# Kernel tuning notes

Measured on AMD Instinct MI355X. Metric: run time of the kernel, lower is better.

Reference implementation:

```python
import jax, jax.numpy as jnp
import numpy as np
from jax import lax

V, H, L, F = 50304, 512, 6, 2048
SKIP_INTERVAL = 1
B, S = 4, 1024


def layer_norm(x, w, b, eps=1e-5):
    mu = jnp.mean(x, axis=-1, keepdims=True)
    var = jnp.mean(jnp.square(x - mu), axis=-1, keepdims=True)
    return (x - mu) * lax.rsqrt(var + eps) * w + b


def setup_inputs() -> dict:
    key = jax.random.key(0)
    ks = jax.random.split(key, 8)
    s = 0.02
    return {
        "input_ids": jax.random.randint(ks[0], (B, S), 0, V, dtype=jnp.int64),
        "embed_in": jax.random.normal(ks[1], (V, H), jnp.float32) * s,
        "hp_w": jax.random.normal(ks[2], (H, H), jnp.float32) * s,
        "hp_b": jnp.zeros((H,), jnp.float32),
        "ln_w": jnp.ones((L, H), jnp.float32),
        "ln_b": jnp.zeros((L, H), jnp.float32),
        "W1": jax.random.normal(ks[3], (L, H, F), jnp.float32) * s,
        "b1": jnp.zeros((L, F), jnp.float32),
        "W2": jax.random.normal(ks[4], (L, F, H), jnp.float32) * s,
        "b2": jnp.zeros((L, H), jnp.float32),
        "ln_f_w": jnp.ones((H,), jnp.float32),
        "ln_f_b": jnp.zeros((H,), jnp.float32),
        "embed_out_w": jax.random.normal(ks[5], (V, H), jnp.float32) * s,
    }


def _stack(h, ln_w, ln_b, W1, b1, W2, b2):
    # scan over L layers; each is pre-LN residual MLP: h + gelu(LN(h) @ W1 + b1) @ W2 + b2
    def step(h, p):
        lw, lb, w1, bb1, w2, bb2 = p
        y = layer_norm(h, lw, lb)
        h = h + jnp.dot(jax.nn.gelu(jnp.dot(y, w1) + bb1), w2) + bb2
        return h, None
    h, _ = lax.scan(step, h, (ln_w, ln_b, W1, b1, W2, b2))
    return h


def reference(input_ids, embed_in, hp_w, hp_b, ln_w, ln_b, W1, b1, W2, b2, ln_f_w, ln_f_b, embed_out_w):
    # forward_selective with attention_mask=None and stateless layers is
    # position-independent, so the token loop vectorizes exactly to [B,S,H].
    h = embed_in[input_ids]  # [B,S,H] gather
    h = _stack(h, ln_w, ln_b, W1, b1, W2, b2)
    for _ in range(SKIP_INTERVAL):
        h = jnp.dot(h, hp_w.T) + hp_b  # hidden_proj
        h = _stack(h, ln_w, ln_b, W1, b1, W2, b2)
    normed = layer_norm(h, ln_f_w, ln_f_b)
    logits = jnp.dot(normed, embed_out_w.T)  # [B,S,V]
    final_hidden = h[:, -1, :]  # [B,H]
    return logits, final_hidden
```

## Files before the change

kernel.cpp:

```cpp
#include <hip/hip_runtime.h>
#include <hip/hip_bf16.h>
#include <cstdint>

using bf16 = __hip_bfloat16;
typedef __bf16 bf16x8 __attribute__((ext_vector_type(8)));
typedef float f32x4 __attribute__((ext_vector_type(4)));

constexpr int Hd = 512;
constexpr int Ld = 6;
constexpr int Fd = 2048;
constexpr int Vd = 50304;
constexpr int Md = 4096;

__device__ __forceinline__ unsigned short f2b(float x) {
  return __builtin_bit_cast(unsigned short, __float2bfloat16(x));
}

__device__ __forceinline__ float gelu_tanh(float x) {
  const float c = 0.7978845608028654f;
  float x3 = x * x * x;
  return 0.5f * x * (1.0f + tanhf(c * (x + 0.044715f * x3)));
}

__device__ __forceinline__ void load16_lds(const bf16* g, bf16* l) {
  __builtin_amdgcn_global_load_lds(
      (const __attribute__((address_space(1))) void*)g,
      (__attribute__((address_space(3))) void*)l, 16, 0, 0);
}

__global__ __launch_bounds__(256) void cast8(const float* __restrict__ in,
                                             bf16* __restrict__ out, int n8) {
  int i = blockIdx.x * 256 + threadIdx.x;
  if (i >= n8) return;
  const float4* p = (const float4*)in;
  float4 a = p[2 * i], b = p[2 * i + 1];
  uint4 o = {(unsigned)f2b(a.x) | ((unsigned)f2b(a.y) << 16),
             (unsigned)f2b(a.z) | ((unsigned)f2b(a.w) << 16),
             (unsigned)f2b(b.x) | ((unsigned)f2b(b.y) << 16),
             (unsigned)f2b(b.z) | ((unsigned)f2b(b.w) << 16)};
  ((uint4*)out)[i] = o;
}

__global__ void transpose_cast(const float* __restrict__ in, bf16* __restrict__ out,
                               int R, int C) {
  __shared__ float tile[32][33];
  int l = blockIdx.z;
  in += (size_t)l * R * C;
  out += (size_t)l * R * C;
  int c0 = blockIdx.x * 32, r0 = blockIdx.y * 32;
#pragma unroll
  for (int i = 0; i < 4; i++) {
    int r = r0 + threadIdx.y + i * 8;
    tile[threadIdx.y + i * 8][threadIdx.x] = in[(size_t)r * C + c0 + threadIdx.x];
  }
  __syncthreads();
#pragma unroll
  for (int i = 0; i < 4; i++) {
    int c = c0 + threadIdx.y + i * 8;
    out[(size_t)c * R + r0 + threadIdx.x] = (bf16)tile[threadIdx.x][threadIdx.y + i * 8];
  }
}

__global__ void gather_embed(const int* __restrict__ ids, const float* __restrict__ emb,
                             float* __restrict__ h) {
  int row = blockIdx.x;
  int id = ids[row];
  const float4* src = (const float4*)(emb + (size_t)id * Hd);
  float4* dst = (float4*)(h + (size_t)row * Hd);
  dst[threadIdx.x] = src[threadIdx.x];
}

template <int MODE>
__global__ __launch_bounds__(256) void ln_rows(
    const float* __restrict__ h, const float* __restrict__ p0,
    const float* __restrict__ p1, const float* __restrict__ fb,
    const float* __restrict__ w, const float* __restrict__ b,
    float* __restrict__ hout, bf16* __restrict__ y) {
  int row = blockIdx.x * 4 + (threadIdx.x >> 6);
  int lane = threadIdx.x & 63;
  size_t base = (size_t)row * Hd + lane * 8;
  float xv[8];
  if constexpr (MODE == 0) {
    *(float4*)&xv[0] = *(const float4*)(h + base);
    *(float4*)&xv[4] = *(const float4*)(h + base + 4);
  } else {
    float4 q0 = *(const float4*)(p0 + base), q1 = *(const float4*)(p0 + base + 4);
    float4 r0 = *(const float4*)(p1 + base), r1 = *(const float4*)(p1 + base + 4);
    float4 f0 = *(const float4*)(fb + lane * 8), f1 = *(const float4*)(fb + lane * 8 + 4);
    xv[0] = q0.x + r0.x + f0.x; xv[1] = q0.y + r0.y + f0.y;
    xv[2] = q0.z + r0.z + f0.z; xv[3] = q0.w + r0.w + f0.w;
    xv[4] = q1.x + r1.x + f1.x; xv[5] = q1.y + r1.y + f1.y;
    xv[6] = q1.z + r1.z + f1.z; xv[7] = q1.w + r1.w + f1.w;
    if constexpr (MODE == 1) {
      float4 a0 = *(const float4*)(h + base), a1 = *(const float4*)(h + base + 4);
      xv[0] += a0.x; xv[1] += a0.y; xv[2] += a0.z; xv[3] += a0.w;
      xv[4] += a1.x; xv[5] += a1.y; xv[6] += a1.z; xv[7] += a1.w;
    }
    *(float4*)(hout + base) = make_float4(xv[0], xv[1], xv[2], xv[3]);
    *(float4*)(hout + base + 4) = make_float4(xv[4], xv[5], xv[6], xv[7]);
  }
  float s = 0.f;
#pragma unroll
  for (int j = 0; j < 8; j++) s += xv[j];
#pragma unroll
  for (int off = 1; off < 64; off <<= 1) s += __shfl_xor(s, off);
  float mu = s * (1.0f / 512.0f);
  float s2 = 0.f;
#pragma unroll
  for (int j = 0; j < 8; j++) {
    xv[j] -= mu;
    s2 += xv[j] * xv[j];
  }
#pragma unroll
  for (int off = 1; off < 64; off <<= 1) s2 += __shfl_xor(s2, off);
  float scale = rsqrtf(s2 * (1.0f / 512.0f) + 1e-5f);
  float o[8];
#pragma unroll
  for (int j = 0; j < 8; j++) {
    float wj = w[lane * 8 + j], bj = b[lane * 8 + j];
    o[j] = xv[j] * scale * wj + bj;
  }
  uint4 pk = {(unsigned)f2b(o[0]) | ((unsigned)f2b(o[1]) << 16),
              (unsigned)f2b(o[2]) | ((unsigned)f2b(o[3]) << 16),
              (unsigned)f2b(o[4]) | ((unsigned)f2b(o[5]) << 16),
              (unsigned)f2b(o[6]) | ((unsigned)f2b(o[7]) << 16)};
  *(uint4*)(y + base) = pk;
}

__global__ __launch_bounds__(256) void finish2(
    const float* __restrict__ p0, const float* __restrict__ p1,
    const float* __restrict__ fb, float* __restrict__ h, bf16* __restrict__ hbf) {
  int i = blockIdx.x * 256 + threadIdx.x;
  size_t base = (size_t)i * 8;
  int col = (int)(base & 511);
  float x[8];
#pragma unroll
  for (int j = 0; j < 8; j += 4) {
    float4 a = *(const float4*)(h + base + j);
    float4 q = *(const float4*)(p0 + base + j);
    float4 r = *(const float4*)(p1 + base + j);
    float4 f = *(const float4*)(fb + col + j);
    x[j] = a.x + q.x + r.x + f.x; x[j + 1] = a.y + q.y + r.y + f.y;
    x[j + 2] = a.z + q.z + r.z + f.z; x[j + 3] = a.w + q.w + r.w + f.w;
    *(float4*)(h + base + j) = make_float4(x[j], x[j + 1], x[j + 2], x[j + 3]);
  }
  uint4 pk = {(unsigned)f2b(x[0]) | ((unsigned)f2b(x[1]) << 16),
              (unsigned)f2b(x[2]) | ((unsigned)f2b(x[3]) << 16),
              (unsigned)f2b(x[4]) | ((unsigned)f2b(x[5]) << 16),
              (unsigned)f2b(x[6]) | ((unsigned)f2b(x[7]) << 16)};
  *(uint4*)(hbf + base) = pk;
}

template <int EPI, int BN, bool MSWZ>
__global__ __launch_bounds__(256) void gemm_bt(
    const bf16* __restrict__ A, const bf16* __restrict__ Bt,
    const float* __restrict__ bias, float* __restrict__ outF,
    bf16* __restrict__ outB, int M, int N, int Klen, int lda, int ldb) {
  constexpr int ASZ = 128 * 32;
  constexpr int BSZ = BN * 32;
  constexpr int TILE = ASZ + BSZ;
  __shared__ bf16 lds[3 * TILE];
  const int tid = threadIdx.x;
  const int wave = tid >> 6;
  const int lane = tid & 63;
  constexpr int NF = BN / 32;
  const int wm = (wave >> 1) * 64;
  const int wn = (wave & 1) * (BN / 2);

  int bm, bn;
  if constexpr (MSWZ) {
    const int per = gridDim.x >> 3;
    const int wg = (blockIdx.x & 7) * per + (blockIdx.x >> 3);
    const int nM = M >> 7;
    bm = wg & (nM - 1);
    bn = wg / nM;
  } else {
    bn = blockIdx.x;
    bm = blockIdx.y;
  }
  const int rowA0 = bm * 128;
  const int rowB0 = bn * BN;
  const int k0 = blockIdx.z * Klen;

  const bf16* srcA[2];
#pragma unroll
  for (int r = 0; r < 2; r++) {
    int c = (r * 4 + wave) * 64 + lane;
    srcA[r] = A + (size_t)(rowA0 + (c >> 2)) * lda + k0 + (c & 3) * 8;
  }
  const bf16* srcB[BN / 64];
#pragma unroll
  for (int r = 0; r < BN / 64; r++) {
    int c = (r * 4 + wave) * 64 + lane;
    srcB[r] = Bt + (size_t)(rowB0 + (c >> 2)) * ldb + k0 + (c & 3) * 8;
  }

  f32x4 acc[4][NF];
#pragma unroll
  for (int i = 0; i < 4; i++)
#pragma unroll
    for (int j = 0; j < NF; j++) acc[i][j] = (f32x4){0.f, 0.f, 0.f, 0.f};

  const int fr = lane & 15;
  const int ko = (lane >> 4) * 8;

  auto STAGE = [&](int slot) {
    bf16* dst = lds + slot * TILE;
#pragma unroll
    for (int r = 0; r < 2; r++) {
      load16_lds(srcA[r], dst + (r * 4 + wave) * 512);
      srcA[r] += 32;
    }
#pragma unroll
    for (int r = 0; r < BN / 64; r++) {
      load16_lds(srcB[r], dst + ASZ + (r * 4 + wave) * 512);
      srcB[r] += 32;
    }
  };

  STAGE(0);
  STAGE(1);
  const int nIter = Klen >> 5;
  int cur = 0, stg = 2;
  for (int it = 0; it < nIter; ++it) {
    if (it < nIter - 1) {
      if constexpr (BN == 64)
        asm volatile("s_waitcnt vmcnt(3)" ::: "memory");
      else
        asm volatile("s_waitcnt vmcnt(4)" ::: "memory");
    } else {
      asm volatile("s_waitcnt vmcnt(0)" ::: "memory");
    }
    __builtin_amdgcn_s_barrier();
    __builtin_amdgcn_sched_barrier(0);
    if (it + 2 < nIter) STAGE(stg);
    const bf16* lA = lds + cur * TILE;
    const bf16* lB = lA + ASZ;
    bf16x8 af[4], bfr[NF];
#pragma unroll
    for (int f = 0; f < 4; f++)
      af[f] = *(const bf16x8*)(lA + (wm + f * 16 + fr) * 32 + ko);
#pragma unroll
    for (int f = 0; f < NF; f++)
      bfr[f] = *(const bf16x8*)(lB + (wn + f * 16 + fr) * 32 + ko);
#pragma unroll
    for (int i = 0; i < 4; i++)
#pragma unroll
      for (int j = 0; j < NF; j++)
        acc[i][j] = __builtin_amdgcn_mfma_f32_16x16x32_bf16(af[i], bfr[j], acc[i][j], 0, 0, 0);
    cur = (cur == 2) ? 0 : cur + 1;
    stg = (stg == 2) ? 0 : stg + 1;
  }

  if constexpr (EPI == 4) outF += (size_t)blockIdx.z * M * N;
  const int orow = (lane >> 4) * 4;
  const int ocol = lane & 15;
#pragma unroll
  for (int i = 0; i < 4; i++) {
#pragma unroll
    for (int j = 0; j < NF; j++) {
      int row0 = rowA0 + wm + i * 16 + orow;
      int col = rowB0 + wn + j * 16 + ocol;
#pragma unroll
      for (int q = 0; q < 4; q++) {
        float v = acc[i][j][q];
        size_t idx = (size_t)(row0 + q) * N + col;
        if constexpr (EPI == 0) {
          outB[idx] = (bf16)gelu_tanh(v + bias[col]);
        } else {
          outF[idx] = v;
        }
      }
    }
  }
}

template <int EPI, bool MSWZ>
__global__ __launch_bounds__(512) void gemm_bt256(
    const bf16* __restrict__ A, const bf16* __restrict__ Bt,
    const float* __restrict__ bias, float* __restrict__ outF,
    bf16* __restrict__ outB, int M, int N, int lda, int ldb) {
  constexpr int ASZ = 256 * 32;
  constexpr int BSZ = 128 * 32;
  constexpr int TILE = ASZ + BSZ;
  __shared__ bf16 lds[3 * TILE];
  const int tid = threadIdx.x;
  const int wave = tid >> 6;
  const int lane = tid & 63;
  const int wm = (wave >> 1) * 64;
  const int wn = (wave & 1) * 64;

  int bm, bn;
  if constexpr (MSWZ) {
    const int per = gridDim.x >> 3;
    const int wg = (blockIdx.x & 7) * per + (blockIdx.x >> 3);
    const int nM = M >> 8;
    bm = wg & (nM - 1);
    bn = wg / nM;
  } else {
    bn = blockIdx.x;
    bm = blockIdx.y;
  }
  const int rowA0 = bm * 256;
  const int rowB0 = bn * 128;

  const bf16* srcA[2];
#pragma unroll
  for (int r = 0; r < 2; r++) {
    int c = r * 512 + tid;
    srcA[r] = A + (size_t)(rowA0 + (c >> 2)) * lda + (c & 3) * 8;
  }
  int cB = tid;
  const bf16* srcB = Bt + (size_t)(rowB0 + (cB >> 2)) * ldb + (cB & 3) * 8;

  f32x4 acc[4][4];
#pragma unroll
  for (int i = 0; i < 4; i++)
#pragma unroll
    for (int j = 0; j < 4; j++) acc[i][j] = (f32x4){0.f, 0.f, 0.f, 0.f};

  const int fr = lane & 15;
  const int ko = (lane >> 4) * 8;

  auto STAGE = [&](int slot) {
    bf16* dst = lds + slot * TILE;
#pragma unroll
    for (int r = 0; r < 2; r++) {
      load16_lds(srcA[r], dst + (r * 512 + tid) * 8);
      srcA[r] += 32;
    }
    load16_lds(srcB, dst + ASZ + tid * 8);
    srcB += 32;
  };

  STAGE(0);
  STAGE(1);
  const int nIter = 512 >> 5;
  int cur = 0, stg = 2;
  for (int it = 0; it < nIter; ++it) {
    if (it < nIter - 1)
      asm volatile("s_waitcnt vmcnt(3)" ::: "memory");
    else
      asm volatile("s_waitcnt vmcnt(0)" ::: "memory");
    __builtin_amdgcn_s_barrier();
    __builtin_amdgcn_sched_barrier(0);
    if (it + 2 < nIter) STAGE(stg);
    const bf16* lA = lds + cur * TILE;
    const bf16* lB = lA + ASZ;
    bf16x8 af[4], bfr[4];
#pragma unroll
    for (int f = 0; f < 4; f++)
      af[f] = *(const bf16x8*)(lA + (wm + f * 16 + fr) * 32 + ko);
#pragma unroll
    for (int f = 0; f < 4; f++)
      bfr[f] = *(const bf16x8*)(lB + (wn + f * 16 + fr) * 32 + ko);
#pragma unroll
    for (int i = 0; i < 4; i++)
#pragma unroll
      for (int j = 0; j < 4; j++)
        acc[i][j] = __builtin_amdgcn_mfma_f32_16x16x32_bf16(af[i], bfr[j], acc[i][j], 0, 0, 0);
    cur = (cur == 2) ? 0 : cur + 1;
    stg = (stg == 2) ? 0 : stg + 1;
  }

  const int orow = (lane >> 4) * 4;
  const int ocol = lane & 15;
#pragma unroll
  for (int i = 0; i < 4; i++) {
#pragma unroll
    for (int j = 0; j < 4; j++) {
      int row0 = rowA0 + wm + i * 16 + orow;
      int col = rowB0 + wn + j * 16 + ocol;
#pragma unroll
      for (int q = 0; q < 4; q++) {
        float v = acc[i][j][q];
        size_t idx = (size_t)(row0 + q) * N + col;
        if constexpr (EPI == 0) {
          outB[idx] = (bf16)gelu_tanh(v + bias[col]);
        } else {
          outF[idx] = v;
        }
      }
    }
  }
}

__global__ void tail_copy(const float* __restrict__ h, float* __restrict__ out) {
  int t = blockIdx.x * 256 + threadIdx.x;
  int b = t >> 9, k = t & 511;
  out[t] = h[((size_t)(b * 1024 + 1023)) * Hd + k];
}

extern "C" void kernel_launch(void* const* d_in, const int* in_sizes, int n_in,
                              void* d_out, int out_size, void* d_ws, size_t ws_size,
                              hipStream_t stream) {
  const int* ids = (const int*)d_in[0];
  const float* emb = (const float*)d_in[1];
  const float* hp_w = (const float*)d_in[2];
  const float* hp_b = (const float*)d_in[3];
  const float* ln_w = (const float*)d_in[4];
  const float* ln_b = (const float*)d_in[5];
  const float* W1 = (const float*)d_in[6];
  const float* b1 = (const float*)d_in[7];
  const float* W2 = (const float*)d_in[8];
  const float* b2 = (const float*)d_in[9];
  const float* lnf_w = (const float*)d_in[10];
  const float* lnf_b = (const float*)d_in[11];
  const float* eow = (const float*)d_in[12];
  float* out = (float*)d_out;

  char* ws = (char*)d_ws;
  float* h = (float*)(ws);
  bf16* ybf = (bf16*)(ws + (8u << 20));
  bf16* abf = (bf16*)(ws + (12u << 20));
  bf16* W1t = (bf16*)(ws + (28u << 20));
  bf16* W2t = (bf16*)(ws + (40u << 20));
  bf16* hpwB = (bf16*)(ws + (52u << 20));
  bf16* eowB = (bf16*)(ws + (53u << 20));

  float* p0 = out;
  float* p1 = out + (size_t)Md * Hd;

  cast8<<<dim3(Vd * Hd / 8 / 256), dim3(256), 0, stream>>>(eow, eowB, Vd * Hd / 8);
  cast8<<<dim3(Hd * Hd / 8 / 256), dim3(256), 0, stream>>>(hp_w, hpwB, Hd * Hd / 8);
  transpose_cast<<<dim3(Fd / 32, Hd / 32, Ld), dim3(32, 8), 0, stream>>>(W1, W1t, Hd, Fd);
  transpose_cast<<<dim3(Hd / 32, Fd / 32, Ld), dim3(32, 8), 0, stream>>>(W2, W2t, Fd, Hd);

  gather_embed<<<dim3(Md), dim3(128), 0, stream>>>(ids, emb, h);

  auto layer = [&](int l, int mode, const float* fb, const float* lw, const float* lb) {
    if (mode == 0)
      ln_rows<0><<<dim3(Md / 4), dim3(256), 0, stream>>>(h, p0, p1, fb, lw, lb, h, ybf);
    else if (mode == 1)
      ln_rows<1><<<dim3(Md / 4), dim3(256), 0, stream>>>(h, p0, p1, fb, lw, lb, h, ybf);
    else
      ln_rows<2><<<dim3(Md / 4), dim3(256), 0, stream>>>(h, p0, p1, fb, lw, lb, h, ybf);
    gemm_bt256<0, false><<<dim3(Fd / 128, Md / 256), dim3(512), 0, stream>>>(
        ybf, W1t + (size_t)l * Fd * Hd, b1 + (size_t)l * Fd, (float*)nullptr, abf,
        Md, Fd, Hd, Hd);
    gemm_bt<4, 64, false><<<dim3(Hd / 64, Md / 128, 2), dim3(256), 0, stream>>>(
        abf, W2t + (size_t)l * Hd * Fd, (const float*)nullptr, p0, (bf16*)nullptr,
        Md, Hd, Fd / 2, Fd, Fd);
  };

  layer(0, 0, nullptr, ln_w, ln_b);
  for (int l = 1; l < Ld; l++)
    layer(l, 1, b2 + (size_t)(l - 1) * Hd, ln_w + (size_t)l * Hd, ln_b + (size_t)l * Hd);
  finish2<<<dim3(Md * Hd / 8 / 256), dim3(256), 0, stream>>>(
      p0, p1, b2 + (size_t)(Ld - 1) * Hd, h, ybf);

  gemm_bt<4, 64, false><<<dim3(Hd / 64, Md / 128, 2), dim3(256), 0, stream>>>(
      ybf, hpwB, (const float*)nullptr, p0, (bf16*)nullptr, Md, Hd, Hd / 2, Hd, Hd);

  layer(0, 2, hp_b, ln_w, ln_b);
  for (int l = 1; l < Ld; l++)
    layer(l, 1, b2 + (size_t)(l - 1) * Hd, ln_w + (size_t)l * Hd, ln_b + (size_t)l * Hd);

  ln_rows<1><<<dim3(Md / 4), dim3(256), 0, stream>>>(
      h, p0, p1, b2 + (size_t)(Ld - 1) * Hd, lnf_w, lnf_b, h, ybf);
  gemm_bt256<3, true><<<dim3((Vd / 128) * (Md / 256)), dim3(512), 0, stream>>>(
      ybf, eowB, (const float*)nullptr, out, (bf16*)nullptr, Md, Vd, Hd, Hd);

  tail_copy<<<dim3(8), dim3(256), 0, stream>>>(h, out + (size_t)Md * Vd);
}
```

Baseline: 1.078 ms.

## Add 256x256-tile logits GEMM with padded vocab and widen W2 GEMM tile

```diff
diff --git a/kernel.cpp b/kernel.cpp
--- a/kernel.cpp
+++ b/kernel.cpp
@@ -10,6 +10,7 @@
 constexpr int Ld = 6;
 constexpr int Fd = 2048;
 constexpr int Vd = 50304;
+constexpr int Vpad = 50432;
 constexpr int Md = 4096;
 
 __device__ __forceinline__ unsigned short f2b(float x) {
@@ -39,6 +40,11 @@
              (unsigned)f2b(b.x) | ((unsigned)f2b(b.y) << 16),
              (unsigned)f2b(b.z) | ((unsigned)f2b(b.w) << 16)};
   ((uint4*)out)[i] = o;
+}
+
+__global__ __launch_bounds__(256) void zero16(bf16* __restrict__ p, int n8) {
+  int i = blockIdx.x * 256 + threadIdx.x;
+  if (i < n8) ((uint4*)p)[i] = uint4{0, 0, 0, 0};
 }
 
 __global__ void transpose_cast(const float* __restrict__ in, bf16* __restrict__ out,
@@ -385,6 +391,102 @@
   }
 }
 
+__global__ __launch_bounds__(512, 1) void gemm_logits(
+    const bf16* __restrict__ A, const bf16* __restrict__ Bt,
+    float* __restrict__ outF, int M, int N, int lda, int ldb) {
+  constexpr int ASZ = 256 * 32;
+  constexpr int BSZ = 256 * 32;
+  constexpr int TILE = ASZ + BSZ;
+  __shared__ bf16 lds[3 * TILE];
+  const int tid = threadIdx.x;
+  const int wave = tid >> 6;
+  const int lane = tid & 63;
+  const int wm = (wave >> 2) * 128;
+  const int wn = (wave & 3) * 64;
+
+  const int per = gridDim.x >> 3;
+  const int wg = (blockIdx.x & 7) * per + (blockIdx.x >> 3);
+  const int bm = wg & 15;
+  const int bn = wg >> 4;
+  const int rowA0 = bm * 256;
+  const int rowB0 = bn * 256;
+
+  const bf16* srcA[2];
+  const bf16* srcB[2];
+#pragma unroll
+  for (int r = 0; r < 2; r++) {
+    int c = r * 512 + tid;
+    srcA[r] = A + (size_t)(rowA0 + (c >> 2)) * lda + (c & 3) * 8;
+    srcB[r] = Bt + (size_t)(rowB0 + (c >> 2)) * ldb + (c & 3) * 8;
+  }
+
+  f32x4 acc[8][4];
+#pragma unroll
+  for (int i = 0; i < 8; i++)
+#pragma unroll
+    for (int j = 0; j < 4; j++) acc[i][j] = (f32x4){0.f, 0.f, 0.f, 0.f};
+
+  const int fr = lane & 15;
+  const int ko = (lane >> 4) * 8;
+
+  auto STAGE = [&](int slot) {
+    bf16* dst = lds + slot * TILE;
+#pragma unroll
+    for (int r = 0; r < 2; r++) {
+      load16_lds(srcA[r], dst + (r * 512 + tid) * 8);
+      srcA[r] += 32;
+      load16_lds(srcB[r], dst + ASZ + (r * 512 + tid) * 8);
+      srcB[r] += 32;
+    }
+  };
+
+  STAGE(0);
+  STAGE(1);
+  const int nIter = 512 >> 5;
+  int cur = 0, stg = 2;
+  for (int it = 0; it < nIter; ++it) {
+    if (it < nIter - 1)
+      asm volatile("s_waitcnt vmcnt(4)" ::: "memory");
+    else
+      asm volatile("s_waitcnt vmcnt(0)" ::: "memory");
+    __builtin_amdgcn_s_barrier();
+    __builtin_amdgcn_sched_barrier(0);
+    if (it + 2 < nIter) STAGE(stg);
+    const bf16* lA = lds + cur * TILE;
+    const bf16* lB = lA + ASZ;
+    bf16x8 af[8], bfr[4];
+#pragma unroll
+    for (int f = 0; f < 8; f++)
+      af[f] = *(const bf16x8*)(lA + (wm + f * 16 + fr) * 32 + ko);
+#pragma unroll
+    for (int f = 0; f < 4; f++)
+      bfr[f] = *(const bf16x8*)(lB + (wn + f * 16 + fr) * 32 + ko);
+#pragma unroll
+    for (int i = 0; i < 8; i++)
+#pragma unroll
+      for (int j = 0; j < 4; j++)
+        acc[i][j] = __builtin_amdgcn_mfma_f32_16x16x32_bf16(af[i], bfr[j], acc[i][j], 0, 0, 0);
+    cur = (cur == 2) ? 0 : cur + 1;
+    stg = (stg == 2) ? 0 : stg + 1;
+  }
+
+  const int orow = (lane >> 4) * 4;
+  const int ocol = lane & 15;
+#pragma unroll
+  for (int i = 0; i < 8; i++) {
+#pragma unroll
+    for (int j = 0; j < 4; j++) {
+      int row0 = rowA0 + wm + i * 16 + orow;
+      int col = rowB0 + wn + j * 16 + ocol;
+      if (col < N) {
+#pragma unroll
+        for (int q = 0; q < 4; q++)
+          outF[(size_t)(row0 + q) * N + col] = acc[i][j][q];
+      }
+    }
+  }
+}
+
 __global__ void tail_copy(const float* __restrict__ h, float* __restrict__ out) {
   int t = blockIdx.x * 256 + threadIdx.x;
   int b = t >> 9, k = t & 511;
@@ -422,6 +524,8 @@
   float* p1 = out + (size_t)Md * Hd;
 
   cast8<<<dim3(Vd * Hd / 8 / 256), dim3(256), 0, stream>>>(eow, eowB, Vd * Hd / 8);
+  zero16<<<dim3((Vpad - Vd) * Hd / 8 / 256), dim3(256), 0, stream>>>(
+      eowB + (size_t)Vd * Hd, (Vpad - Vd) * Hd / 8);
   cast8<<<dim3(Hd * Hd / 8 / 256), dim3(256), 0, stream>>>(hp_w, hpwB, Hd * Hd / 8);
   transpose_cast<<<dim3(Fd / 32, Hd / 32, Ld), dim3(32, 8), 0, stream>>>(W1, W1t, Hd, Fd);
   transpose_cast<<<dim3(Hd / 32, Fd / 32, Ld), dim3(32, 8), 0, stream>>>(W2, W2t, Fd, Hd);
@@ -438,7 +542,7 @@
     gemm_bt256<0, false><<<dim3(Fd / 128, Md / 256), dim3(512), 0, stream>>>(
         ybf, W1t + (size_t)l * Fd * Hd, b1 + (size_t)l * Fd, (float*)nullptr, abf,
         Md, Fd, Hd, Hd);
-    gemm_bt<4, 64, false><<<dim3(Hd / 64, Md / 128, 2), dim3(256), 0, stream>>>(
+    gemm_bt<4, 128, false><<<dim3(Hd / 128, Md / 128, 2), dim3(256), 0, stream>>>(
         abf, W2t + (size_t)l * Hd * Fd, (const float*)nullptr, p0, (bf16*)nullptr,
         Md, Hd, Fd / 2, Fd, Fd);
   };
@@ -449,7 +553,7 @@
   finish2<<<dim3(Md * Hd / 8 / 256), dim3(256), 0, stream>>>(
       p0, p1, b2 + (size_t)(Ld - 1) * Hd, h, ybf);
 
-  gemm_bt<4, 64, false><<<dim3(Hd / 64, Md / 128, 2), dim3(256), 0, stream>>>(
+  gemm_bt<4, 128, false><<<dim3(Hd / 128, Md / 128, 2), dim3(256), 0, stream>>>(
       ybf, hpwB, (const float*)nullptr, p0, (bf16*)nullptr, Md, Hd, Hd / 2, Hd, Hd);
 
   layer(0, 2, hp_b, ln_w, ln_b);
@@ -458,8 +562,8 @@
 
   ln_rows<1><<<dim3(Md / 4), dim3(256), 0, stream>>>(
       h, p0, p1, b2 + (size_t)(Ld - 1) * Hd, lnf_w, lnf_b, h, ybf);
-  gemm_bt256<3, true><<<dim3((Vd / 128) * (Md / 256)), dim3(512), 0, stream>>>(
-      ybf, eowB, (const float*)nullptr, out, (bf16*)nullptr, Md, Vd, Hd, Hd);
+  gemm_logits<<<dim3((Vpad / 256) * (Md / 256)), dim3(512), 0, stream>>>(
+      ybf, eowB, out, Md, Vd, Hd, Hd);
 
   tail_copy<<<dim3(8), dim3(256), 0, stream>>>(h, out + (size_t)Md * Vd);
 }
```

After: 984.1 us. -8.7%, faster.
